# Kernel tuning notes

Measured on AMD Instinct MI355X. Metric: run time of the kernel, lower is better.

The kernel has to match this reference:

```python
import jax, jax.numpy as jnp
import numpy as np

N_SAMPLES = 2 ** 15  # 32768
NYQUIST = 22050.0 / 2.0
MIN_FREQ = 40.0 / NYQUIST
MAX_FREQ = 4000.0 / NYQUIST
FREQ_RANGE = MAX_FREQ - MIN_FREQ


def interp_linear(x, out_size):
    """torch F.interpolate(mode='linear', align_corners=False) along last axis."""
    in_size = x.shape[-1]
    scale = in_size / out_size
    coords = (jnp.arange(out_size, dtype=x.dtype) + 0.5) * scale - 0.5
    coords = jnp.clip(coords, 0.0, in_size - 1)
    lo = jnp.floor(coords).astype(jnp.int32)
    hi = jnp.minimum(lo + 1, in_size - 1)
    w = coords - lo.astype(x.dtype)
    return x[..., lo] * (1.0 - w) + x[..., hi] * w


def translate(pair, shift, scale):
    # angle of complex(pair[:,:,0], pair[:,:,1]) / pi, then affine
    angle = jnp.arctan2(pair[:, :, 1, :], pair[:, :, 0, :]) / np.pi
    return shift + angle * scale


def setup_inputs() -> dict:
    key = jax.random.key(0)
    k1, k2 = jax.random.split(key)
    x = jax.random.normal(k1, (16, 8, 10, 128), dtype=jnp.float32)
    noise = jax.random.normal(k2, (16, 8, N_SAMPLES), dtype=jnp.float32)
    return {"x": x, "noise": noise}


def reference(x, noise):
    # x: (batch, n_osc, 10, time_ctrl); noise: (batch, n_osc, N_SAMPLES)
    basic = x[:, :, 0:2, :]
    amp = jnp.sqrt(jnp.sum(basic * basic, axis=2))            # (b, o, t)
    amp = interp_linear(amp, N_SAMPLES)                       # (b, o, N)

    f0 = translate(basic, MIN_FREQ, FREQ_RANGE)               # control-rate
    mix = interp_linear(translate(x[:, :, 2:4, :], 1.0, 0.5), N_SAMPLES)
    harm_amp = amp * mix
    noise_amp = amp * (1.0 - mix)

    noise_std = translate(x[:, :, 4:6, :], MIN_FREQ, FREQ_RANGE)
    mod_factor = translate(x[:, :, 6:8, :], 0.25, 4.75)
    b = translate(x[:, :, 8:10, :], 0.1, 9.9)

    # band_filtered_noise: narrowband noise as a frequency-jittered sine
    f0_fr = interp_linear(f0, N_SAMPLES)
    std_fr = interp_linear(noise_std, N_SAMPLES)
    bfn = jnp.sin(jnp.cumsum(f0_fr + noise * std_fr, axis=-1))
    noise_sig = noise_amp * bfn

    mod_factor = interp_linear(mod_factor, N_SAMPLES)
    b = interp_linear(b, N_SAMPLES)
    mod = b * jnp.sin(jnp.cumsum(mod_factor, axis=-1))
    sig = harm_amp * jnp.sin(jnp.cumsum(f0_fr, axis=-1) + mod)

    mixed = noise_sig + sig                                   # (b, o, N)
    return jnp.mean(mixed, axis=1, keepdims=True)             # (b, 1, N)
```

## Files before the change

kernel.cpp:

```cpp
#include <hip/hip_runtime.h>
#include <math.h>

#define NS     32768
#define NB     128
#define CELL   32
#define CPB    32
#define PART   (CELL * CPB)
#define NPARTS (NS / PART)
#define TPB    256
#define NBATCH 16
#define GRID   (NBATCH * NPARTS)
#define NBIN   6

__device__ __forceinline__ float sinr(float x) {
    return __builtin_amdgcn_sinf(x - rintf(x));
}

__device__ __forceinline__ void seg_params(int i, int& lo, int& hi,
                                           double& w0, double& wst) {
    if (i < 128)            { lo = 0;   hi = 1;   w0 = 0.0; wst = 0.0; }
    else if (i >= NS - 128) { lo = 127; hi = 127; w0 = 0.0; wst = 0.0; }
    else {
        lo = (i - 128) >> 8;  hi = lo + 1;
        int off = (i - 128) & 255;
        w0 = (off + 0.5) * (1.0 / 256.0);
        wst = 1.0 / 256.0;
    }
}

__device__ __forceinline__ double bin_value(const float* xs, int q, int j) {
    const double PI_    = 3.14159265358979323846;
    const double INV2PI = 0.15915494309189533576888376337251;
    const double MINF   = 40.0 / 11025.0;
    const double FRNG   = (4000.0 - 40.0) / 11025.0;
    if (q == 0) {
        double a0 = (double)xs[j], a1 = (double)xs[NB + j];
        return sqrt(a0 * a0 + a1 * a1);
    }
    double ang = atan2((double)xs[(2 * q - 1) * NB + j],
                       (double)xs[(2 * q - 2) * NB + j]) / PI_;
    double sh, sc;
    if      (q == 1) { sh = MINF; sc = FRNG; }
    else if (q == 2) { sh = 1.0;  sc = 0.5;  }
    else if (q == 3) { sh = MINF; sc = FRNG; }
    else if (q == 4) { sh = 0.25; sc = 4.75; }
    else             { sh = 0.1;  sc = 9.9;  }
    double v = sh + ang * sc;
    if (q != 2) v *= INV2PI;
    return v;
}

__device__ __forceinline__ void cell_totals(
        const float4* nn, double f0L, double dF0, double stL, double dSt,
        double mfL, double dMf, double w0, double wst,
        double& t1, double& t3, double& t2) {
    float s0 = 0.f, s1 = 0.f;
    #pragma unroll
    for (int q4 = 0; q4 < CELL / 4; ++q4) {
        float4 nv = nn[q4];
        float jd = (float)(q4 * 4);
        s0 += nv.x; s1 = fmaf(jd, nv.x, s1);
        s0 += nv.y; s1 = fmaf(jd + 1.f, nv.y, s1);
        s0 += nv.z; s1 = fmaf(jd + 2.f, nv.z, s1);
        s0 += nv.w; s1 = fmaf(jd + 3.f, nv.w, s1);
    }
    double S0 = (double)s0, S1 = (double)s1;
    double sw = 32.0 * w0 + 496.0 * wst;
    t3 = 32.0 * f0L + dF0 * sw;
    t2 = 32.0 * mfL + dMf * sw;
    t1 = t3 + stL * S0 + dSt * (w0 * S0 + wst * S1);
}

__global__ __launch_bounds__(TPB)
void span_kernel(const float* __restrict__ xg, const float* __restrict__ ng,
                 double* __restrict__ wspan) {
    __shared__ double binsA[8][3][NBIN];

    int bx = blockIdx.x, bb = bx >> 5, p = bx & (NPARTS - 1);
    int tid = threadIdx.x, lane = tid & 63;
    int h = tid >> 5, c = tid & 31;
    int P = p * PART;
    int b0 = (P - 128) >> 8; if (b0 < 0) b0 = 0;
    int s  = (bb << 3) + h;
    int i0 = P + c * CELL;

    if (tid < 144) {
        int j = tid % NBIN, r = (tid / NBIN) % 3, h2 = tid / (3 * NBIN);
        int q = (r == 0) ? 1 : (r == 1) ? 3 : 4;
        const float* xs = xg + (size_t)((bb << 3) + h2) * 10 * NB;
        binsA[h2][r][j] = bin_value(xs, q, min(b0 + j, NB - 1));
    }
    __syncthreads();

    int lo, hi; double w0, wst;
    seg_params(i0, lo, hi, w0, wst);
    int jL = lo - b0, jH = hi - b0;
    double f0L = binsA[h][0][jL], dF0 = binsA[h][0][jH] - f0L;
    double stL = binsA[h][1][jL], dSt = binsA[h][1][jH] - stL;
    double mfL = binsA[h][2][jL], dMf = binsA[h][2][jH] - mfL;

    const float4* nn = reinterpret_cast<const float4*>(ng + (size_t)s * NS + i0);
    double t1, t3, t2;
    cell_totals(nn, f0L, dF0, stL, dSt, mfL, dMf, w0, wst, t1, t3, t2);

    double v1 = t1, v3 = t3, v2 = t2;
    #pragma unroll
    for (int d = 1; d < 32; d <<= 1) {
        double u1 = __shfl_up(v1, d);
        double u3 = __shfl_up(v3, d);
        double u2 = __shfl_up(v2, d);
        if ((lane & 31) >= d) { v1 += u1; v3 += u3; v2 += u2; }
    }
    if (c == 31) {
        size_t sb = ((size_t)s * NPARTS + p) * 3;
        wspan[sb + 0] = v1; wspan[sb + 1] = v3; wspan[sb + 2] = v2;
    }
}

__global__ __launch_bounds__(TPB)
void fm_kernel(const float* __restrict__ xg, const float* __restrict__ ng,
               const double* __restrict__ wspan, float* __restrict__ out) {
    __shared__ double binsA[8][3][NBIN];
    __shared__ float  binsB[8][6][NBIN];
    __shared__ double wtot[4][8][3];
    __shared__ double prefL[8][3];

    int bx = blockIdx.x, bb = bx >> 5, p = bx & (NPARTS - 1);
    int tid = threadIdx.x, lane = tid & 63, wid = tid >> 6;
    int h = tid & 7, c = tid >> 3;
    int P = p * PART;
    int b0 = (P - 128) >> 8; if (b0 < 0) b0 = 0;
    int s  = (bb << 3) + h;
    int i0 = P + c * CELL;

    if (tid < 192) {
        int r = tid & 7, g = tid >> 3, k = g % 3, h2 = g / 3;
        const double* sp = wspan + ((size_t)(((bb << 3) + h2) * NPARTS)) * 3 + k;
        double acc = 0.0;
        #pragma unroll
        for (int q = 0; q < NPARTS / 8; ++q) {
            int idx = r + q * 8;
            if (idx < p) acc += sp[idx * 3];
        }
        #pragma unroll
        for (int m = 1; m <= 4; m <<= 1) acc += __shfl_xor(acc, m);
        if (r == 0) prefL[h2][k] = acc;
    }
    for (int idx = tid; idx < 8 * 6 * NBIN; idx += TPB) {
        int j = idx % NBIN, q = (idx / NBIN) % 6, h2 = idx / (6 * NBIN);
        const float* xs = xg + (size_t)((bb << 3) + h2) * 10 * NB;
        double v = bin_value(xs, q, min(b0 + j, NB - 1));
        binsB[h2][q][j] = (float)v;
        if      (q == 1) binsA[h2][0][j] = v;
        else if (q == 3) binsA[h2][1][j] = v;
        else if (q == 4) binsA[h2][2][j] = v;
    }
    __syncthreads();

    int lo, hi; double w0, wst;
    seg_params(i0, lo, hi, w0, wst);
    int jL = lo - b0, jH = hi - b0;
    double f0L = binsA[h][0][jL], dF0 = binsA[h][0][jH] - f0L;
    double stL = binsA[h][1][jL], dSt = binsA[h][1][jH] - stL;
    double mfL = binsA[h][2][jL], dMf = binsA[h][2][jH] - mfL;

    const float4* nn = reinterpret_cast<const float4*>(ng + (size_t)s * NS + i0);
    double t1, t3, t2;
    cell_totals(nn, f0L, dF0, stL, dSt, mfL, dMf, w0, wst, t1, t3, t2);

    double v1 = t1, v3 = t3, v2 = t2;
    #pragma unroll
    for (int d = 8; d < 64; d <<= 1) {
        double u1 = __shfl_up(v1, d);
        double u3 = __shfl_up(v3, d);
        double u2 = __shfl_up(v2, d);
        if (lane >= d) { v1 += u1; v3 += u3; v2 += u2; }
    }
    if (lane >= 56) { wtot[wid][h][0] = v1; wtot[wid][h][1] = v3; wtot[wid][h][2] = v2; }
    __syncthreads();
    double b1 = 0.0, b3 = 0.0, b2 = 0.0;
    #pragma unroll
    for (int k = 0; k < 3; ++k)
        if (wid > k) { b1 += wtot[k][h][0]; b3 += wtot[k][h][1]; b2 += wtot[k][h][2]; }

    double a1 = prefL[h][0] + b1 + (v1 - t1);
    double a3 = prefL[h][1] + b3 + (v3 - t3);
    double a2 = prefL[h][2] + b2 + (v2 - t2);
    float fr1 = (float)(a1 - rint(a1));
    float fr3 = (float)(a3 - rint(a3));
    float fr2 = (float)(a2 - rint(a2));

    float amL = binsB[h][0][jL], dAm = binsB[h][0][jH] - amL;
    float g0L = binsB[h][1][jL], gF0 = binsB[h][1][jH] - g0L;
    float mxL = binsB[h][2][jL], dMx = binsB[h][2][jH] - mxL;
    float gsL = binsB[h][3][jL], gSt = binsB[h][3][jH] - gsL;
    float gmL = binsB[h][4][jL], gMf = binsB[h][4][jH] - gmL;
    float bbL = binsB[h][5][jL], dBb = binsB[h][5][jH] - bbL;
    float w0f = (float)w0, wsf = (float)wst;

    float arr[CELL];
    float d1 = 0.f, d2 = 0.f, d3 = 0.f;
    #pragma unroll
    for (int q4 = 0; q4 < CELL / 4; ++q4) {
        float4 nv = nn[q4];
        float nf[4] = {nv.x, nv.y, nv.z, nv.w};
        #pragma unroll
        for (int u = 0; u < 4; ++u) {
            int j = q4 * 4 + u;
            float wf  = fmaf((float)j, wsf, w0f);
            float f0v = fmaf(wf, gF0, g0L);
            float stv = fmaf(wf, gSt, gsL);
            float mfv = fmaf(wf, gMf, gmL);
            d3 += f0v;
            d1 += fmaf(nf[u], stv, f0v);
            d2 += mfv;
            float ampv = fmaf(wf, dAm, amL);
            float mixv = fmaf(wf, dMx, mxL);
            float bv   = fmaf(wf, dBb, bbL);
            float s2 = sinr(fr2 + d2);
            float s1 = sinr(fr1 + d1);
            float s3 = sinr(fmaf(bv, s2, fr3 + d3));
            float harm = ampv * mixv;
            arr[j] = fmaf(harm, s3, (ampv - harm) * s1);
        }
    }

    #pragma unroll
    for (int m = 1; m <= 4; m <<= 1) {
        #pragma unroll
        for (int j = 0; j < CELL; ++j) arr[j] += __shfl_xor(arr[j], m);
    }
    if (h == 0) {
        float4* op = reinterpret_cast<float4*>(out + (size_t)bb * NS + i0);
        #pragma unroll
        for (int j4 = 0; j4 < CELL / 4; ++j4)
            op[j4] = make_float4(arr[j4 * 4 + 0] * 0.125f, arr[j4 * 4 + 1] * 0.125f,
                                 arr[j4 * 4 + 2] * 0.125f, arr[j4 * 4 + 3] * 0.125f);
    }
}

extern "C" void kernel_launch(void* const* d_in, const int* in_sizes, int n_in,
                              void* d_out, int out_size, void* d_ws, size_t ws_size,
                              hipStream_t stream) {
    const float* x     = (const float*)d_in[0];
    const float* noise = (const float*)d_in[1];
    float* out = (float*)d_out;
    double* wspan = (double*)d_ws;
    span_kernel<<<GRID, TPB, 0, stream>>>(x, noise, wspan);
    fm_kernel<<<GRID, TPB, 0, stream>>>(x, noise, wspan, out);
}
```

Baseline: 80.62 us.

## Fuse span and FM kernels into one launch with flag-based decoupled lookback

```diff
diff --git a/kernel.cpp b/kernel.cpp
--- a/kernel.cpp
+++ b/kernel.cpp
@@ -9,7 +9,8 @@
 #define NPARTS (NS / PART)
 #define TPB    256
 #define NBATCH 16
-#define GRID   (NBATCH * NPARTS)
+#define PGRID  (NBATCH * NPARTS)
+#define GRID   (2 * PGRID)
 #define NBIN   6
 
 __device__ __forceinline__ float sinr(float x) {
@@ -72,80 +73,71 @@
 }
 
 __global__ __launch_bounds__(TPB)
-void span_kernel(const float* __restrict__ xg, const float* __restrict__ ng,
-                 double* __restrict__ wspan) {
-    __shared__ double binsA[8][3][NBIN];
-
-    int bx = blockIdx.x, bb = bx >> 5, p = bx & (NPARTS - 1);
-    int tid = threadIdx.x, lane = tid & 63;
-    int h = tid >> 5, c = tid & 31;
-    int P = p * PART;
-    int b0 = (P - 128) >> 8; if (b0 < 0) b0 = 0;
-    int s  = (bb << 3) + h;
-    int i0 = P + c * CELL;
-
-    if (tid < 144) {
-        int j = tid % NBIN, r = (tid / NBIN) % 3, h2 = tid / (3 * NBIN);
-        int q = (r == 0) ? 1 : (r == 1) ? 3 : 4;
-        const float* xs = xg + (size_t)((bb << 3) + h2) * 10 * NB;
-        binsA[h2][r][j] = bin_value(xs, q, min(b0 + j, NB - 1));
-    }
-    __syncthreads();
-
-    int lo, hi; double w0, wst;
-    seg_params(i0, lo, hi, w0, wst);
-    int jL = lo - b0, jH = hi - b0;
-    double f0L = binsA[h][0][jL], dF0 = binsA[h][0][jH] - f0L;
-    double stL = binsA[h][1][jL], dSt = binsA[h][1][jH] - stL;
-    double mfL = binsA[h][2][jL], dMf = binsA[h][2][jH] - mfL;
-
-    const float4* nn = reinterpret_cast<const float4*>(ng + (size_t)s * NS + i0);
-    double t1, t3, t2;
-    cell_totals(nn, f0L, dF0, stL, dSt, mfL, dMf, w0, wst, t1, t3, t2);
-
-    double v1 = t1, v3 = t3, v2 = t2;
-    #pragma unroll
-    for (int d = 1; d < 32; d <<= 1) {
-        double u1 = __shfl_up(v1, d);
-        double u3 = __shfl_up(v3, d);
-        double u2 = __shfl_up(v2, d);
-        if ((lane & 31) >= d) { v1 += u1; v3 += u3; v2 += u2; }
-    }
-    if (c == 31) {
-        size_t sb = ((size_t)s * NPARTS + p) * 3;
-        wspan[sb + 0] = v1; wspan[sb + 1] = v3; wspan[sb + 2] = v2;
-    }
-}
-
-__global__ __launch_bounds__(TPB)
-void fm_kernel(const float* __restrict__ xg, const float* __restrict__ ng,
-               const double* __restrict__ wspan, float* __restrict__ out) {
+void fm_fused_kernel(const float* __restrict__ xg, const float* __restrict__ ng,
+                     double* __restrict__ wspan, int* __restrict__ wflag,
+                     float* __restrict__ out) {
     __shared__ double binsA[8][3][NBIN];
     __shared__ float  binsB[8][6][NBIN];
     __shared__ double wtot[4][8][3];
     __shared__ double prefL[8][3];
 
-    int bx = blockIdx.x, bb = bx >> 5, p = bx & (NPARTS - 1);
+    int bx0 = blockIdx.x;
+    bool producer = bx0 < PGRID;
+    int bx = producer ? bx0 : bx0 - PGRID;
+    int bb = bx >> 5, p = bx & (NPARTS - 1);
     int tid = threadIdx.x, lane = tid & 63, wid = tid >> 6;
-    int h = tid & 7, c = tid >> 3;
     int P = p * PART;
     int b0 = (P - 128) >> 8; if (b0 < 0) b0 = 0;
+
+    if (producer) {
+        int h = tid >> 5, c = tid & 31;
+        int s  = (bb << 3) + h;
+        int i0 = P + c * CELL;
+
+        if (tid < 144) {
+            int j = tid % NBIN, r = (tid / NBIN) % 3, h2 = tid / (3 * NBIN);
+            int q = (r == 0) ? 1 : (r == 1) ? 3 : 4;
+            const float* xs = xg + (size_t)((bb << 3) + h2) * 10 * NB;
+            binsA[h2][r][j] = bin_value(xs, q, min(b0 + j, NB - 1));
+        }
+        __syncthreads();
+
+        int lo, hi; double w0, wst;
+        seg_params(i0, lo, hi, w0, wst);
+        int jL = lo - b0, jH = hi - b0;
+        double f0L = binsA[h][0][jL], dF0 = binsA[h][0][jH] - f0L;
+        double stL = binsA[h][1][jL], dSt = binsA[h][1][jH] - stL;
+        double mfL = binsA[h][2][jL], dMf = binsA[h][2][jH] - mfL;
+
+        const float4* nn = reinterpret_cast<const float4*>(ng + (size_t)s * NS + i0);
+        double t1, t3, t2;
+        cell_totals(nn, f0L, dF0, stL, dSt, mfL, dMf, w0, wst, t1, t3, t2);
+
+        double v1 = t1, v3 = t3, v2 = t2;
+        #pragma unroll
+        for (int d = 1; d < 32; d <<= 1) {
+            double u1 = __shfl_up(v1, d);
+            double u3 = __shfl_up(v3, d);
+            double u2 = __shfl_up(v2, d);
+            if ((lane & 31) >= d) { v1 += u1; v3 += u3; v2 += u2; }
+        }
+        if (c == 31) {
+            size_t sb = ((size_t)s * NPARTS + p) * 3;
+            __hip_atomic_store(&wspan[sb + 0], v1, __ATOMIC_RELAXED, __HIP_MEMORY_SCOPE_AGENT);
+            __hip_atomic_store(&wspan[sb + 1], v3, __ATOMIC_RELAXED, __HIP_MEMORY_SCOPE_AGENT);
+            __hip_atomic_store(&wspan[sb + 2], v2, __ATOMIC_RELAXED, __HIP_MEMORY_SCOPE_AGENT);
+        }
+        __syncthreads();
+        if (tid == 0)
+            __hip_atomic_store(&wflag[bb * NPARTS + p], 1,
+                               __ATOMIC_RELEASE, __HIP_MEMORY_SCOPE_AGENT);
+        return;
+    }
+
+    int h = tid & 7, c = tid >> 3;
     int s  = (bb << 3) + h;
     int i0 = P + c * CELL;
 
-    if (tid < 192) {
-        int r = tid & 7, g = tid >> 3, k = g % 3, h2 = g / 3;
-        const double* sp = wspan + ((size_t)(((bb << 3) + h2) * NPARTS)) * 3 + k;
-        double acc = 0.0;
-        #pragma unroll
-        for (int q = 0; q < NPARTS / 8; ++q) {
-            int idx = r + q * 8;
-            if (idx < p) acc += sp[idx * 3];
-        }
-        #pragma unroll
-        for (int m = 1; m <= 4; m <<= 1) acc += __shfl_xor(acc, m);
-        if (r == 0) prefL[h2][k] = acc;
-    }
     for (int idx = tid; idx < 8 * 6 * NBIN; idx += TPB) {
         int j = idx % NBIN, q = (idx / NBIN) % 6, h2 = idx / (6 * NBIN);
         const float* xs = xg + (size_t)((bb << 3) + h2) * 10 * NB;
@@ -183,9 +175,35 @@
     for (int k = 0; k < 3; ++k)
         if (wid > k) { b1 += wtot[k][h][0]; b3 += wtot[k][h][1]; b2 += wtot[k][h][2]; }
 
-    double a1 = prefL[h][0] + b1 + (v1 - t1);
-    double a3 = prefL[h][1] + b3 + (v3 - t3);
-    double a2 = prefL[h][2] + b2 + (v2 - t2);
+    double e1 = b1 + v1 - t1, e3 = b3 + v3 - t3, e2 = b2 + v2 - t2;
+
+    if (tid < NPARTS) {
+        while (__hip_atomic_load(&wflag[bb * NPARTS + tid], __ATOMIC_ACQUIRE,
+                                 __HIP_MEMORY_SCOPE_AGENT) == 0)
+            __builtin_amdgcn_s_sleep(2);
+    }
+    __syncthreads();
+
+    if (tid < 192) {
+        int r = tid & 7, g = tid >> 3, k = g % 3, h2 = g / 3;
+        const double* sp = wspan + ((size_t)(((bb << 3) + h2) * NPARTS)) * 3 + k;
+        double acc = 0.0;
+        #pragma unroll
+        for (int q = 0; q < NPARTS / 8; ++q) {
+            int idx = r + q * 8;
+            if (idx < p)
+                acc += __hip_atomic_load(&sp[idx * 3], __ATOMIC_RELAXED,
+                                         __HIP_MEMORY_SCOPE_AGENT);
+        }
+        #pragma unroll
+        for (int m = 1; m <= 4; m <<= 1) acc += __shfl_xor(acc, m);
+        if (r == 0) prefL[h2][k] = acc;
+    }
+    __syncthreads();
+
+    double a1 = prefL[h][0] + e1;
+    double a3 = prefL[h][1] + e3;
+    double a2 = prefL[h][2] + e2;
     float fr1 = (float)(a1 - rint(a1));
     float fr3 = (float)(a3 - rint(a3));
     float fr2 = (float)(a2 - rint(a2));
@@ -246,6 +264,7 @@
     const float* noise = (const float*)d_in[1];
     float* out = (float*)d_out;
     double* wspan = (double*)d_ws;
-    span_kernel<<<GRID, TPB, 0, stream>>>(x, noise, wspan);
-    fm_kernel<<<GRID, TPB, 0, stream>>>(x, noise, wspan, out);
-}
+    int*    wflag = (int*)(wspan + (size_t)128 * NPARTS * 3);
+    hipMemsetAsync(wflag, 0, NBATCH * NPARTS * sizeof(int), stream);
+    fm_fused_kernel<<<GRID, TPB, 0, stream>>>(x, noise, wspan, wflag, out);
+}
```

After: 86.50 us. 1.07x slower.
